# Optimization experiments

Hardware: AMD Instinct MI355X
Metric: run time of the kernel (lower is better)

Reference implementation:

```python
import jax, jax.numpy as jnp
import numpy as np
import math

E = 512; V = 8192; B = 32; T = 16; L = 4; FF = 2048; NH = 8; TEMP = 1.0


def setup_inputs() -> dict:
    key = jax.random.key(0)
    ks = jax.random.split(key, 16)
    s = 0.02
    nrm = lambda k, shape, sc=s: jax.random.normal(k, shape, jnp.float32) * sc
    d = {}
    d['encoder_state'] = nrm(ks[0], (1, B, E), 1.0)
    d['special_symbol'] = nrm(ks[1], (1, 1, E))
    d['embed_weight'] = nrm(ks[2], (V, E), E ** -0.5)
    d['out_w'] = nrm(ks[3], (V, E))
    d['out_b'] = jnp.zeros((V,), jnp.float32)
    u = jax.random.uniform(ks[4], (T, B, V), jnp.float32, 1e-6, 1.0 - 1e-6)
    d['gumbel'] = -jnp.log(-jnp.log(u))
    d['sa_qkv_w'] = nrm(ks[5], (L, 3 * E, E)); d['sa_qkv_b'] = jnp.zeros((L, 3 * E), jnp.float32)
    d['sa_out_w'] = nrm(ks[6], (L, E, E)); d['sa_out_b'] = jnp.zeros((L, E), jnp.float32)
    d['ca_qkv_w'] = nrm(ks[7], (L, 3 * E, E)); d['ca_qkv_b'] = jnp.zeros((L, 3 * E), jnp.float32)
    d['ca_out_w'] = nrm(ks[8], (L, E, E)); d['ca_out_b'] = jnp.zeros((L, E), jnp.float32)
    for i in (1, 2, 3):
        d['ln%d_g' % i] = jnp.ones((L, E), jnp.float32)
        d['ln%d_b' % i] = jnp.zeros((L, E), jnp.float32)
    d['w1'] = nrm(ks[9], (L, FF, E)); d['b1'] = jnp.zeros((L, FF), jnp.float32)
    d['w2'] = nrm(ks[10], (L, E, FF)); d['b2'] = jnp.zeros((L, E), jnp.float32)
    return d


def _ln(x, g, b):
    m = x.mean(-1, keepdims=True)
    v = ((x - m) ** 2).mean(-1, keepdims=True)
    return (x - m) / jnp.sqrt(v + 1e-5) * g + b


def _mha(q_in, kv_in, qkv_w, qkv_b, out_w, out_b, mask):
    # q_in: [Sq,B,E], kv_in: [Sk,B,E]; fused PyTorch-style in_proj
    hd = E // NH
    wq, wk, wv = jnp.split(qkv_w, 3, 0)
    bq, bk, bv = jnp.split(qkv_b, 3, 0)
    q = (q_in @ wq.T + bq).reshape(q_in.shape[0], -1, NH, hd)
    k = (kv_in @ wk.T + bk).reshape(kv_in.shape[0], -1, NH, hd)
    v = (kv_in @ wv.T + bv).reshape(kv_in.shape[0], -1, NH, hd)
    s = jnp.einsum('qbhd,kbhd->bhqk', q, k) / math.sqrt(hd)
    if mask is not None:
        s = s + mask
    a = jax.nn.softmax(s, -1)
    o = jnp.einsum('bhqk,kbhd->qbhd', a, v).reshape(q_in.shape[0], -1, E)
    return o @ out_w.T + out_b


def _forward(encoder_state, special_symbol, embed_weight, out_w, out_b, gumbel,
             sa_qkv_w, sa_qkv_b, sa_out_w, sa_out_b,
             ca_qkv_w, ca_qkv_b, ca_out_w, ca_out_b,
             ln1_g, ln1_b, ln2_g, ln2_b, ln3_g, ln3_b,
             w1, b1, w2, b2):
    bsz = encoder_state.shape[1]
    embed_scale = math.sqrt(E)
    inp = jnp.broadcast_to(special_symbol, (1, bsz, E))  # special start symbol
    seq_steps, distribs = [], []
    for step in range(T):
        t = step + 1
        mask = jnp.where(jnp.triu(jnp.ones((t, t), bool), 1), -jnp.inf, 0.0)
        x = inp
        for l in range(L):  # post-norm TransformerDecoderLayer, erf-gelu
            sa = _mha(x, x, sa_qkv_w[l], sa_qkv_b[l], sa_out_w[l], sa_out_b[l], mask)
            x = _ln(x + sa, ln1_g[l], ln1_b[l])
            ca = _mha(x, encoder_state, ca_qkv_w[l], ca_qkv_b[l], ca_out_w[l], ca_out_b[l], None)
            x = _ln(x + ca, ln2_g[l], ln2_b[l])
            ff = jax.nn.gelu(x @ w1[l].T + b1[l], approximate=False) @ w2[l].T + b2[l]
            x = _ln(x + ff, ln3_g[l], ln3_b[l])
        logits = x[-1] @ out_w.T + out_b  # [B,V], last position only
        distribs.append(jax.nn.softmax(logits, -1))
        sample = jax.nn.softmax((logits + gumbel[step]) / TEMP, -1)  # gumbel-softmax (training mode)
        seq_steps.append(sample)
        new_emb = (sample @ embed_weight) * embed_scale  # soft embedding lookup
        inp = jnp.concatenate([inp, new_emb[None]], 0)
    sequence = jnp.stack(seq_steps).transpose(1, 0, 2)  # [B,T,V]
    eos = jnp.zeros_like(sequence[:, :1, :]).at[:, :, 0].set(1.0)
    sequence = jnp.concatenate([sequence, eos], 1)  # [B,T+1,V]
    return sequence, jnp.stack(distribs)  # distribs: [T,B,V]


def reference(encoder_state, special_symbol, embed_weight, out_w, out_b, gumbel,
              sa_qkv_w, sa_qkv_b, sa_out_w, sa_out_b,
              ca_qkv_w, ca_qkv_b, ca_out_w, ca_out_b,
              ln1_g, ln1_b, ln2_g, ln2_b, ln3_g, ln3_b,
              w1, b1, w2, b2):
    return _forward(encoder_state, special_symbol, embed_weight, out_w, out_b, gumbel,
                    sa_qkv_w, sa_qkv_b, sa_out_w, sa_out_b,
                    ca_qkv_w, ca_qkv_b, ca_out_w, ca_out_b,
                    ln1_g, ln1_b, ln2_g, ln2_b, ln3_g, ln3_b,
                    w1, b1, w2, b2)
```

## Files before the change

### kernel.cpp

```cpp
#include <hip/hip_runtime.h>
#include <math.h>

#define BB 32
#define EE 512
#define VV 8192
#define TT 16
#define LL 4
#define FFD 2048
#define NHD 8
#define HDD 64
#define LDP 520
#define RWP 516
#define OLP 72
#define SCALE_EMB 22.627416997969522f

typedef __attribute__((ext_vector_type(8))) short bf16x8;
typedef __attribute__((ext_vector_type(4))) float f32x4;
typedef unsigned long long ull;

__device__ __forceinline__ f32x4 mfma16(bf16x8 a, bf16x8 b, f32x4 c){
  return __builtin_amdgcn_mfma_f32_16x16x32_bf16(a, b, c, 0, 0, 0);
}

__device__ __forceinline__ float wave_sum(float v){
// ... 35 lines not shown
        wt[(kk+2)*68 + fr] = v.z;
        wt[(kk+3)*68 + fr] = v.w;
      }
    }
    __syncthreads();
    const unsigned short* xr0 = xs + (bg*2)*EE + k0;
    const unsigned short* xr1 = xr0 + EE;
    #pragma unroll 8
    for (int k = 0; k < 64; k += 2){
      float w0[4], w1[4];
      *(float4*)w0 = *(const float4*)(wt + (k+0)*68 + fg*4);
      *(float4*)w1 = *(const float4*)(wt + (k+1)*68 + fg*4);
      float2 xv0 = bf2_to_f2(xr0 + k);
      float2 xv1 = bf2_to_f2(xr1 + k);
      #pragma unroll
      for (int i = 0; i < 4; ++i){
        acc[i][0] += w0[i]*xv0.x + w1[i]*xv0.y;
        acc[i][1] += w0[i]*xv1.x + w1[i]*xv1.y;
      }
    }
  }
}

__device__ __forceinline__ void stage_x_p(unsigned short* xs,
    const float* __restrict__ xraw, const float* __restrict__ ybuf,
    const float* __restrict__ g, const float* __restrict__ bt, int use_ln,
    float* __restrict__ xlnout){
  if (!use_ln){
    for (int i = threadIdx.x; i < BB*EE; i += 256){
      int r = i >> 9, c = i & 511;
      xs[r*LDP + c] = f_to_bf(xraw[i]);
    }
  } else {
    const int lane = threadIdx.x & 63, wv = threadIdx.x >> 6;
    for (int r = wv*8; r < wv*8 + 8; ++r){
      float vals[8]; float s = 0.f, s2 = 0.f;
      #pragma unroll
      for (int j = 0; j < 8; ++j){
        float v = ybuf[r*EE + lane + j*64];
        vals[j] = v; s += v; s2 += v*v;
      }
      s = wave_sum(s); s2 = wave_sum(s2);
      float m = s * (1.f/EE);
      float inv = rsqrtf(s2*(1.f/EE) - m*m + 1e-5f);
      #pragma unroll
      for (int j = 0; j < 8; ++j){
        int c = lane + j*64;
        float v = (vals[j]-m)*inv*g[c] + bt[c];
        xs[r*LDP + c] = f_to_bf(v);
        if (xlnout) xlnout[r*EE + c] = v;
      }
    }
  }
  __syncthreads();
}


__global__ __launch_bounds__(256) void k_init(const float* __restrict__ special,
    float* __restrict__ dseq, float* __restrict__ x, float* __restrict__ o2){
  int idx = blockIdx.x*256 + threadIdx.x;
  if (idx < BB*VV){
    int b = idx >> 13, v = idx & (VV-1);
    dseq[(size_t)b*((TT+1)*VV) + (size_t)TT*VV + v] = (v == 0) ? 1.f : 0.f;
  } else if (idx < BB*VV + BB*EE){
    int i = idx - BB*VV;
    x[i] = special[i & (EE-1)];
  } else if (idx < BB*VV + 2*BB*EE){
    o2[idx - BB*VV - BB*EE] = 0.f;
  }
}

__global__ __launch_bounds__(256) void k_penc(const float* __restrict__ enc,
    const float* __restrict__ w, const float* __restrict__ bias, float* __restrict__ venc){
  __shared__ unsigned short xs[BB*EE];
  __shared__ float wt[64*68];
  const int l = blockIdx.x >> 3, et = blockIdx.x & 7;
  for (int i = threadIdx.x; i < BB*EE; i += 256) xs[i] = f_to_bf(enc[i]);
  const int t = threadIdx.x, fg = t & 15, bg = t >> 4;
  const int f0 = et*64;
  const float* wl = w + (size_t)l*3*EE*EE + (size_t)(2*EE + f0)*EE;
  const float* bl = bias + l*3*EE + 2*EE + f0;
  float acc[4][2];
  #pragma unroll
  for (int i = 0; i < 4; ++i){ float bv = bl[fg*4+i]; acc[i][0] = bv; acc[i][1] = bv; }
  gemm_chunk(wl, EE, xs, wt, acc);
  #pragma unroll
  for (int i = 0; i < 4; ++i)
    #pragma unroll
    for (int j = 0; j < 2; ++j)
      venc[(size_t)l*BB*EE + (bg*2+j)*EE + f0 + fg*4 + i] = acc[i][j];
}
// ... 28 lines not shown
    ushort4 o;
    o.x = f_to_bf(v.x); o.y = f_to_bf(v.y); o.z = f_to_bf(v.z); o.w = f_to_bf(v.w);
    ((ushort4*)d)[i] = o;
  }
}

__global__ __launch_bounds__(256) void k_embT(const float* __restrict__ emb,
    unsigned short* __restrict__ eT){
  __shared__ unsigned short tl[64][68];
  const int vt = blockIdx.x >> 3, et = blockIdx.x & 7;
  const int v0 = vt*64, e0 = et*64;
  for (int i = threadIdx.x; i < 64*64; i += 256){
    int vv = i >> 6, ee = i & 63;
    tl[vv][ee] = f_to_bf(emb[(size_t)(v0+vv)*EE + e0 + ee]);
  }
  __syncthreads();
  for (int i = threadIdx.x; i < 64*64; i += 256){
    int ee = i >> 6, vv = i & 63;
    eT[(size_t)(e0+ee)*VV + v0 + vv] = tl[vv][ee];
  }
}


__global__ __launch_bounds__(256) void k_A(
    const float* __restrict__ x, const float* __restrict__ ybuf,
    const float* __restrict__ lng, const float* __restrict__ lnb, int use_ln,
    const unsigned short* __restrict__ Wb, const float* __restrict__ bias,
    const unsigned short* __restrict__ owb_l,
    float* __restrict__ kcl, float* __restrict__ vcl,
    float* __restrict__ xln, float* __restrict__ o2,
    int tpos, int tlen){
  __shared__ unsigned short xs[BB*LDP];
  __shared__ __align__(16) float qs[BB*68];
  __shared__ float att[BB*16];
  const int h = blockIdx.x;
  stage_x_p(xs, x, ybuf, lng, lnb, use_ln, (use_ln && h == 0) ? xln : nullptr);
  const int t = threadIdx.x, wv = t >> 6, lane = t & 63;
  const int lm = lane & 15, kg = lane >> 4;
  const unsigned short* b0r = xs + lm*LDP + kg*8;
  const unsigned short* b1r = xs + (lm+16)*LDP + kg*8;
  #pragma unroll
  for (int c = 0; c < 3; ++c){
    const int fbase = c*EE + h*64 + wv*16;
    const unsigned short* ar = Wb + (size_t)(fbase + lm)*EE + kg*8;
    f32x4 acc0 = {0.f,0.f,0.f,0.f}, acc1 = {0.f,0.f,0.f,0.f};
    #pragma unroll 4
    for (int ks = 0; ks < 16; ++ks){
      bf16x8 a  = *reinterpret_cast<const bf16x8*>(ar + ks*32);
      bf16x8 b0 = *reinterpret_cast<const bf16x8*>(b0r + ks*32);
      bf16x8 b1 = *reinterpret_cast<const bf16x8*>(b1r + ks*32);
      acc0 = mfma16(a, b0, acc0);
      acc1 = mfma16(a, b1, acc1);
    }
    #pragma unroll
    for (int r = 0; r < 4; ++r){
      const int frel = wv*16 + kg*4 + r;
      const float bv = bias[c*EE + h*64 + frel];
      float v0 = acc0[r] + bv, v1 = acc1[r] + bv;
      if (c == 0){
        qs[lm*68 + frel] = v0;
        qs[(lm+16)*68 + frel] = v1;
      } else if (c == 1){
        kcl[((lm*NHD + h)*TT + tpos)*HDD + frel] = v0;
        kcl[(((lm+16)*NHD + h)*TT + tpos)*HDD + frel] = v1;
      } else {
        vcl[((lm*NHD + h)*TT + tpos)*HDD + frel] = v0;
        vcl[(((lm+16)*NHD + h)*TT + tpos)*HDD + frel] = v1;
      }
    }
  }
  __syncthreads();
  #pragma unroll
  for (int pp = 0; pp < 2; ++pp){
    const int p = t + pp*256;
    const int b = p >> 4, j = p & 15;
    if (j < tlen){
      const float* qrow = qs + b*68;
      const float* krow = kcl + ((b*NHD + h)*TT + j)*HDD;
      float a = 0.f;
      #pragma unroll
      for (int d = 0; d < HDD; d += 4){
        float4 qv = *(const float4*)(qrow + d);
        float4 kv = *(const float4*)(krow + d);
        a += qv.x*kv.x + qv.y*kv.y + qv.z*kv.z + qv.w*kv.w;
      }
      att[b*16 + j] = a*0.125f;
    }
  }
  __syncthreads();
  if (t < 32){
    const int b = t;
    float m = -1e30f;
    for (int j = 0; j < tlen; ++j) m = fmaxf(m, att[b*16 + j]);
    float s = 0.f;
    for (int j = 0; j < tlen; ++j) s += __expf(att[b*16 + j] - m);
    float inv = 1.f/s;
    for (int j = 0; j < tlen; ++j) att[b*16 + j] = __expf(att[b*16 + j] - m)*inv;
  }
  __syncthreads();
  unsigned short* o_lds = (unsigned short*)qs;
  {
    const int b = t >> 3, d0 = (t & 7)*8;
    float acc[8];
    #pragma unroll
    for (int i = 0; i < 8; ++i) acc[i] = 0.f;
    const float* vrow = vcl + ((b*NHD + h)*TT)*HDD + d0;
    for (int j = 0; j < tlen; ++j){
      const float a = att[b*16 + j];
      float4 v0 = *(const float4*)(vrow + j*HDD);
      float4 v1 = *(const float4*)(vrow + j*HDD + 4);
      acc[0] += a*v0.x; acc[1] += a*v0.y; acc[2] += a*v0.z; acc[3] += a*v0.w;
      acc[4] += a*v1.x; acc[5] += a*v1.y; acc[6] += a*v1.z; acc[7] += a*v1.w;
    }
    *(ull*)(o_lds + b*OLP + d0)     = pkbf4(acc[0], acc[1], acc[2], acc[3]);
    *(ull*)(o_lds + b*OLP + d0 + 4) = pkbf4(acc[4], acc[5], acc[6], acc[7]);
  }
  __syncthreads();
  const unsigned short* ob0 = o_lds + lm*OLP + kg*8;
  const unsigned short* ob1 = o_lds + (lm+16)*OLP + kg*8;
  #pragma unroll
  for (int ft = 0; ft < 8; ++ft){
    const int f0 = wv*128 + ft*16;
    const unsigned short* ar = owb_l + (size_t)(f0 + lm)*EE + h*HDD + kg*8;
    f32x4 a0 = {0.f,0.f,0.f,0.f}, a1 = {0.f,0.f,0.f,0.f};
    #pragma unroll
    for (int ks = 0; ks < 2; ++ks){
      bf16x8 a  = *reinterpret_cast<const bf16x8*>(ar + ks*32);
      bf16x8 x0 = *reinterpret_cast<const bf16x8*>(ob0 + ks*32);
      bf16x8 x1 = *reinterpret_cast<const bf16x8*>(ob1 + ks*32);
      a0 = mfma16(a, x0, a0);
      a1 = mfma16(a, x1, a1);
    }
    #pragma unroll
    for (int r = 0; r < 4; ++r){
      const int f = f0 + kg*4 + r;
      atomicAdd(&o2[lm*EE + f], a0[r]);
      atomicAdd(&o2[(lm+16)*EE + f], a1[r]);
    }
  }
}

__global__ __launch_bounds__(256) void k_B(
    const float* __restrict__ o2, const float* __restrict__ resid,
    const float* __restrict__ ob, const float* __restrict__ cac,
    const float* __restrict__ g1, const float* __restrict__ b1g,
    const float* __restrict__ g2, const float* __restrict__ b2g,
    const float* __restrict__ b2bias,
    const unsigned short* __restrict__ w1b, const float* __restrict__ b1bias,
    unsigned short* __restrict__ Hb, float* __restrict__ ybuf){
  __shared__ unsigned short xs[BB*LDP];
  __shared__ __align__(16) float rawf[BB*RWP];
  const int t = threadIdx.x, blk = blockIdx.x;
  for (int i = t*4; i < BB*EE; i += 1024){
    const int r = i >> 9, c = i & 511;
    float4 a  = *(const float4*)(o2 + i);
    float4 rr = *(const float4*)(resid + i);
    float4 ov = *(const float4*)(ob + c);
    rawf[r*RWP + c]     = a.x + rr.x + ov.x;
    rawf[r*RWP + c + 1] = a.y + rr.y + ov.y;
    rawf[r*RWP + c + 2] = a.z + rr.z + ov.z;
    rawf[r*RWP + c + 3] = a.w + rr.w + ov.w;
  }
  __syncthreads();
  const int wv = t >> 6, lane = t & 63;
  const int lm = lane & 15, kg = lane >> 4;
  {
    float* yi = (blk == 0) ? ybuf : nullptr;
    const int c0 = lane*4, c1 = 256 + lane*4;
    for (int r = wv*8; r < wv*8 + 8; ++r){
      float v[8];
      *(float4*)(v+0) = *(const float4*)(rawf + r*RWP + c0);
      *(float4*)(v+4) = *(const float4*)(rawf + r*RWP + c1);
      float s = 0.f, s2 = 0.f;
      #pragma unroll
      for (int j = 0; j < 8; ++j){ s += v[j]; s2 += v[j]*v[j]; }
      s = wave_sum(s); s2 = wave_sum(s2);
      float m = s*(1.f/EE), inv = rsqrtf(s2*(1.f/EE) - m*m + 1e-5f);
      float4 ca0 = *(const float4*)(cac + (size_t)r*EE + c0);
      float4 ca1 = *(const float4*)(cac + (size_t)r*EE + c1);
      float nv[8]; float u = 0.f, u2 = 0.f;
      nv[0] = (v[0]-m)*inv*g1[c0+0] + b1g[c0+0] + ca0.x;
      nv[1] = (v[1]-m)*inv*g1[c0+1] + b1g[c0+1] + ca0.y;
      nv[2] = (v[2]-m)*inv*g1[c0+2] + b1g[c0+2] + ca0.z;
      nv[3] = (v[3]-m)*inv*g1[c0+3] + b1g[c0+3] + ca0.w;
      nv[4] = (v[4]-m)*inv*g1[c1+0] + b1g[c1+0] + ca1.x;
      nv[5] = (v[5]-m)*inv*g1[c1+1] + b1g[c1+1] + ca1.y;
      nv[6] = (v[6]-m)*inv*g1[c1+2] + b1g[c1+2] + ca1.z;
      nv[7] = (v[7]-m)*inv*g1[c1+3] + b1g[c1+3] + ca1.w;
      #pragma unroll
      for (int j = 0; j < 8; ++j){ u += nv[j]; u2 += nv[j]*nv[j]; }
      u = wave_sum(u); u2 = wave_sum(u2);
      float m2 = u*(1.f/EE), inv2 = rsqrtf(u2*(1.f/EE) - m2*m2 + 1e-5f);
      float o0 = (nv[0]-m2)*inv2*g2[c0+0] + b2g[c0+0];
      float o1 = (nv[1]-m2)*inv2*g2[c0+1] + b2g[c0+1];
      float o2v = (nv[2]-m2)*inv2*g2[c0+2] + b2g[c0+2];
      float o3 = (nv[3]-m2)*inv2*g2[c0+3] + b2g[c0+3];
      float o4 = (nv[4]-m2)*inv2*g2[c1+0] + b2g[c1+0];
      float o5 = (nv[5]-m2)*inv2*g2[c1+1] + b2g[c1+1];
      float o6 = (nv[6]-m2)*inv2*g2[c1+2] + b2g[c1+2];
      float o7 = (nv[7]-m2)*inv2*g2[c1+3] + b2g[c1+3];
      *(ull*)(xs + r*LDP + c0) = pkbf4(o0, o1, o2v, o3);
      *(ull*)(xs + r*LDP + c1) = pkbf4(o4, o5, o6, o7);
      if (yi){
        float4 w0, w1;
        w0.x = o0 + b2bias[c0+0]; w0.y = o1 + b2bias[c0+1];
        w0.z = o2v + b2bias[c0+2]; w0.w = o3 + b2bias[c0+3];
        w1.x = o4 + b2bias[c1+0]; w1.y = o5 + b2bias[c1+1];
        w1.z = o6 + b2bias[c1+2]; w1.w = o7 + b2bias[c1+3];
        *(float4*)(yi + (size_t)r*EE + c0) = w0;
        *(float4*)(yi + (size_t)r*EE + c1) = w1;
      }
    }
    __syncthreads();
  }
  {
    const int f0w = blk*64 + wv*16;
    const unsigned short* ar = w1b + (size_t)(f0w + lm)*EE + kg*8;
    const unsigned short* b0r = xs + lm*LDP + kg*8;
    const unsigned short* b1r = xs + (lm+16)*LDP + kg*8;
    f32x4 acc0 = {0.f,0.f,0.f,0.f}, acc1 = {0.f,0.f,0.f,0.f};
    #pragma unroll 4
    for (int ks = 0; ks < 16; ++ks){
      bf16x8 a  = *reinterpret_cast<const bf16x8*>(ar + ks*32);
      bf16x8 b0 = *reinterpret_cast<const bf16x8*>(b0r + ks*32);
      bf16x8 b1 = *reinterpret_cast<const bf16x8*>(b1r + ks*32);
      acc0 = mfma16(a, b0, acc0);
      acc1 = mfma16(a, b1, acc1);
    }
    const int fb = f0w + kg*4;
    float h0[4], h1[4];
    #pragma unroll
    for (int r = 0; r < 4; ++r){
      const float bv = b1bias[fb + r];
      float v0 = acc0[r] + bv, v1 = acc1[r] + bv;
      h0[r] = 0.5f*v0*(1.f + erff(v0*0.70710678118654752f));
      h1[r] = 0.5f*v1*(1.f + erff(v1*0.70710678118654752f));
    }
    *(ull*)(Hb + lm*FFD + fb)      = pkbf4(h0[0], h0[1], h0[2], h0[3]);
    *(ull*)(Hb + (lm+16)*FFD + fb) = pkbf4(h1[0], h1[1], h1[2], h1[3]);
  }
}

__global__ __launch_bounds__(256) void k_C(
    const unsigned short* __restrict__ Hb, const unsigned short* __restrict__ w2b,
    float* __restrict__ ybuf, float* __restrict__ o2z){
  __shared__ unsigned short xs[BB*LDP];
  const int t = threadIdx.x, blk = blockIdx.x;
  const int k0 = (blk >> 3)*512;
  for (int i = t*16; i < BB*512; i += 4096){
    int r = i >> 9, c = i & 511;
    const unsigned short* s = Hb + (size_t)r*FFD + k0 + c;
    ull* dst = (ull*)(xs + r*LDP + c);
    dst[0] = *(const ull*)s;      dst[1] = *(const ull*)(s+4);
    dst[2] = *(const ull*)(s+8);  dst[3] = *(const ull*)(s+12);
  }
  __syncthreads();
  const int wv = t >> 6, lane = t & 63;
  const int lm = lane & 15, kg = lane >> 4;
  const int f0w = (blk & 7)*64 + wv*16;
  const unsigned short* ar = w2b + (size_t)(f0w + lm)*FFD + k0 + kg*8;
  const unsigned short* b0r = xs + lm*LDP + kg*8;
  const unsigned short* b1r = xs + (lm+16)*LDP + kg*8;
  f32x4 acc0 = {0.f,0.f,0.f,0.f}, acc1 = {0.f,0.f,0.f,0.f};
  #pragma unroll 4
  for (int ks = 0; ks < 16; ++ks){
    bf16x8 a  = *reinterpret_cast<const bf16x8*>(ar + ks*32);
    bf16x8 b0 = *reinterpret_cast<const bf16x8*>(b0r + ks*32);
    bf16x8 b1 = *reinterpret_cast<const bf16x8*>(b1r + ks*32);
    acc0 = mfma16(a, b0, acc0);
    acc1 = mfma16(a, b1, acc1);
  }
  #pragma unroll
  for (int r = 0; r < 4; ++r){
    const int f = f0w + kg*4 + r;
    atomicAdd(&ybuf[lm*EE + f], acc0[r]);
    atomicAdd(&ybuf[(lm+16)*EE + f], acc1[r]);
  }
  float2 z; z.x = 0.f; z.y = 0.f;
  *(float2*)(o2z + blk*512 + t*2) = z;
}

__global__ __launch_bounds__(256) void k_logits_m(
    const float* __restrict__ ybuf, const float* __restrict__ lng, const float* __restrict__ lnb,
    const unsigned short* __restrict__ Wb, const float* __restrict__ bias,
    float* __restrict__ logits){
  __shared__ unsigned short xs[BB*LDP];
  stage_x_p(xs, nullptr, ybuf, lng, lnb, 1, nullptr);
  const int t = threadIdx.x, w = t >> 6, l = t & 63;
  const int lm = l & 15, kg = l >> 4;
  const int f0w = blockIdx.x*64 + w*16;
  const unsigned short* ar = Wb + (size_t)(f0w + lm)*EE + kg*8;
  const unsigned short* b0r = xs + lm*LDP + kg*8;
  const unsigned short* b1r = xs + (lm+16)*LDP + kg*8;
  f32x4 acc0 = {0.f,0.f,0.f,0.f}, acc1 = {0.f,0.f,0.f,0.f};
  #pragma unroll 4
  for (int ks = 0; ks < 16; ++ks){
    bf16x8 a  = *reinterpret_cast<const bf16x8*>(ar + ks*32);
    bf16x8 b0 = *reinterpret_cast<const bf16x8*>(b0r + ks*32);
    bf16x8 b1 = *reinterpret_cast<const bf16x8*>(b1r + ks*32);
    acc0 = mfma16(a, b0, acc0);
    acc1 = mfma16(a, b1, acc1);
  }
  #pragma unroll
  for (int r = 0; r < 4; ++r){
    const int f = f0w + kg*4 + r;
    const float bv = bias[f];
    logits[lm*VV + f]      = acc0[r] + bv;
    logits[(lm+16)*VV + f] = acc1[r] + bv;
  }
}

__global__ __launch_bounds__(256) void k_softmax(const float* __restrict__ logits,
    const float* __restrict__ gum, float* __restrict__ dseq, float* __restrict__ ddist,
    unsigned short* __restrict__ sbf, float* __restrict__ x, int step){
  const int b = blockIdx.x, t = threadIdx.x, lane = t & 63, wv = t >> 6;
  __shared__ float red[8];
  const float* lr = logits + (size_t)b*VV;
  const float* gr = gum + (size_t)b*VV;
  float m1 = -1e30f, m2 = -1e30f;
  for (int i = t; i < VV; i += 256){
    float l = lr[i];
    m1 = fmaxf(m1, l);
    m2 = fmaxf(m2, l + gr[i]);
  }
  for (int o = 32; o; o >>= 1){ m1 = fmaxf(m1, __shfl_down(m1,o)); m2 = fmaxf(m2, __shfl_down(m2,o)); }
  if (lane == 0){ red[wv] = m1; red[4+wv] = m2; }
  __syncthreads();
  m1 = fmaxf(fmaxf(red[0],red[1]), fmaxf(red[2],red[3]));
  m2 = fmaxf(fmaxf(red[4],red[5]), fmaxf(red[6],red[7]));
  __syncthreads();
  float s1 = 0.f, s2 = 0.f;
  for (int i = t; i < VV; i += 256){
    float l = lr[i];
    s1 += __expf(l - m1);
    s2 += __expf(l + gr[i] - m2);
  }
  for (int o = 32; o; o >>= 1){ s1 += __shfl_down(s1,o); s2 += __shfl_down(s2,o); }
  if (lane == 0){ red[wv] = s1; red[4+wv] = s2; }
  __syncthreads();
  s1 = red[0]+red[1]+red[2]+red[3];
  s2 = red[4]+red[5]+red[6]+red[7];
  float r1 = 1.f/s1, r2 = 1.f/s2;
  float* dq = dseq + (size_t)b*((TT+1)*VV) + (size_t)step*VV;
  float* dd = ddist + (size_t)b*VV;
  for (int i = t; i < VV; i += 256){
    float l = lr[i];
    dd[i] = __expf(l - m1)*r1;
    float qv = __expf(l + gr[i] - m2)*r2;
    dq[i] = qv;
    sbf[(size_t)b*VV + i] = f_to_bf(qv);
  }
  for (int i = t; i < EE; i += 256) x[b*EE + i] = 0.f;
}

__global__ __launch_bounds__(256) void k_embed_m(
    const unsigned short* __restrict__ eT, const unsigned short* __restrict__ sbf,
    float* __restrict__ x){
  const int t = threadIdx.x, w = t >> 6, l = t & 63;
  const int lm = l & 15, kg = l >> 4;
  const int e0w = (blockIdx.x & 7)*64 + w*16;
  const int v0 = (blockIdx.x >> 3)*1024;
  const unsigned short* ar  = eT + (size_t)(e0w + lm)*VV + v0 + kg*8;
  const unsigned short* b0r = sbf + (size_t)lm*VV + v0 + kg*8;
  const unsigned short* b1r = sbf + (size_t)(lm+16)*VV + v0 + kg*8;
  f32x4 acc0 = {0.f,0.f,0.f,0.f}, acc1 = {0.f,0.f,0.f,0.f};
  #pragma unroll 8
  for (int ks = 0; ks < 32; ++ks){
    bf16x8 a  = *reinterpret_cast<const bf16x8*>(ar + ks*32);
    bf16x8 b0 = *reinterpret_cast<const bf16x8*>(b0r + ks*32);
    bf16x8 b1 = *reinterpret_cast<const bf16x8*>(b1r + ks*32);
    acc0 = mfma16(a, b0, acc0);
    acc1 = mfma16(a, b1, acc1);
  }
  #pragma unroll
  for (int r = 0; r < 4; ++r){
    const int e = e0w + kg*4 + r;
    atomicAdd(&x[lm*EE + e], acc0[r]*SCALE_EMB);
    atomicAdd(&x[(lm+16)*EE + e], acc1[r]*SCALE_EMB);
  }
}

extern "C" void kernel_launch(void* const* d_in, const int* in_sizes, int n_in,
                              void* d_out, int out_size, void* d_ws, size_t ws_size,
                              hipStream_t stream){
  (void)in_sizes; (void)n_in; (void)out_size; (void)ws_size;
  const float* enc  = (const float*)d_in[0];
  const float* spec = (const float*)d_in[1];
  const float* embw = (const float*)d_in[2];
  const float* outw = (const float*)d_in[3];
  const float* outb = (const float*)d_in[4];
  const float* gumb = (const float*)d_in[5];
  const float* saqw = (const float*)d_in[6];
  const float* saqb = (const float*)d_in[7];
  const float* saow = (const float*)d_in[8];
  const float* saob = (const float*)d_in[9];
  const float* caqw = (const float*)d_in[10];
  const float* caqb = (const float*)d_in[11];
  const float* caow = (const float*)d_in[12];
  const float* caob = (const float*)d_in[13];
  const float* l1g  = (const float*)d_in[14];
  const float* l1b  = (const float*)d_in[15];
  const float* l2g  = (const float*)d_in[16];
  const float* l2b  = (const float*)d_in[17];
  const float* l3g  = (const float*)d_in[18];
  const float* l3b  = (const float*)d_in[19];
  const float* w1   = (const float*)d_in[20];
  const float* b1   = (const float*)d_in[21];
  const float* w2   = (const float*)d_in[22];
  const float* b2   = (const float*)d_in[23];

  float* dout = (float*)d_out;
  float* dseq = dout;
  float* ddistbase = dout + (size_t)BB*(TT+1)*VV;

  unsigned char* p = (unsigned char*)d_ws;
  auto alloc = [&](size_t bytes) -> void* {
    void* r = (void*)p; p += (bytes + 255) & ~(size_t)255; return r;
  };
  float* x      = (float*)alloc(BB*EE*4);
  float* y      = (float*)alloc(BB*EE*4);
  float* xln    = (float*)alloc(BB*EE*4);
  float* o2     = (float*)alloc(BB*EE*4);
  float* logits = (float*)alloc((size_t)BB*VV*4);
  float* venc   = (float*)alloc((size_t)LL*BB*EE*4);
  float* cac    = (float*)alloc((size_t)LL*BB*EE*4);
  float* kcache = (float*)alloc((size_t)LL*BB*EE*TT*4);
  float* vcache = (float*)alloc((size_t)LL*BB*EE*TT*4);
  unsigned short* Hb    = (unsigned short*)alloc(BB*FFD*2);
  unsigned short* sbf   = (unsigned short*)alloc((size_t)BB*VV*2);
  unsigned short* wqkvb = (unsigned short*)alloc((size_t)LL*3*EE*EE*2);
  unsigned short* owb   = (unsigned short*)alloc((size_t)LL*EE*EE*2);
  unsigned short* w1b   = (unsigned short*)alloc((size_t)LL*FFD*EE*2);
  unsigned short* w2b   = (unsigned short*)alloc((size_t)LL*FFD*EE*2);
  unsigned short* outwb = (unsigned short*)alloc((size_t)VV*EE*2);
  unsigned short* eTb   = (unsigned short*)alloc((size_t)EE*VV*2);

  k_init<<<1152, 256, 0, stream>>>(spec, dseq, x, o2);
  k_penc<<<32, 256, 0, stream>>>(enc, caqw, caqb, venc);
  k_pca<<<32, 256, 0, stream>>>(venc, caow, caob, cac);
  k_cvt<<<(LL*3*EE*EE/4 + 255)/256, 256, 0, stream>>>(saqw, wqkvb, LL*3*EE*EE/4);
  k_cvt<<<(LL*EE*EE/4 + 255)/256, 256, 0, stream>>>(saow, owb, LL*EE*EE/4);
  k_cvt<<<(LL*FFD*EE/4 + 255)/256, 256, 0, stream>>>(w1, w1b, LL*FFD*EE/4);
  k_cvt<<<(LL*FFD*EE/4 + 255)/256, 256, 0, stream>>>(w2, w2b, LL*FFD*EE/4);
  k_cvt<<<(VV*EE/4 + 255)/256, 256, 0, stream>>>(outw, outwb, VV*EE/4);
  k_embT<<<1024, 256, 0, stream>>>(embw, eTb);

  for (int step = 0; step < TT; ++step){
    const int tpos = step, tlen = step + 1;
    for (int l = 0; l < LL; ++l){
      const int use_ln = (l > 0);
      const float* lg = l3g + (use_ln ? (l-1)*EE : 0);
      const float* lb = l3b + (use_ln ? (l-1)*EE : 0);
      float* kcl = kcache + (size_t)l*BB*EE*TT;
      float* vcl = vcache + (size_t)l*BB*EE*TT;
      const float* resid = use_ln ? xln : x;
      k_A<<<NHD, 256, 0, stream>>>(x, y, lg, lb, use_ln,
          wqkvb + (size_t)l*3*EE*EE, saqb + (size_t)l*3*EE,
          owb + (size_t)l*EE*EE, kcl, vcl, xln, o2, tpos, tlen);
      k_B<<<32, 256, 0, stream>>>(o2, resid, saob + (size_t)l*EE,
          cac + (size_t)l*BB*EE,
          l1g + l*EE, l1b + l*EE, l2g + l*EE, l2b + l*EE, b2 + l*EE,
          w1b + (size_t)l*FFD*EE, b1 + l*FFD, Hb, y);
      k_C<<<32, 256, 0, stream>>>(Hb, w2b + (size_t)l*EE*FFD, y, o2);
    }
    k_logits_m<<<128, 256, 0, stream>>>(y, l3g + 3*EE, l3b + 3*EE, outwb, outb, logits);
    k_softmax<<<32, 256, 0, stream>>>(logits, gumb + (size_t)step*BB*VV, dseq,
        ddistbase + (size_t)step*BB*VV, sbf, x, step);
    k_embed_m<<<64, 256, 0, stream>>>(eTb, sbf, x);
  }
}
```

Before: 4.543 ms.

## Fuse FFN kernels into one, double-buffer y/o2, and widen blocks to 512 threads

```diff
diff --git a/kernel.cpp b/kernel.cpp
--- a/kernel.cpp
+++ b/kernel.cpp
@@ -81,18 +81,19 @@
   }
 }
 
-__device__ __forceinline__ void stage_x_p(unsigned short* xs,
+__device__ __forceinline__ void stage_x_512(unsigned short* xs,
     const float* __restrict__ xraw, const float* __restrict__ ybuf,
     const float* __restrict__ g, const float* __restrict__ bt, int use_ln,
     float* __restrict__ xlnout){
   if (!use_ln){
-    for (int i = threadIdx.x; i < BB*EE; i += 256){
+    for (int i = threadIdx.x*4; i < BB*EE; i += 2048){
+      float4 v = *(const float4*)(xraw + i);
       int r = i >> 9, c = i & 511;
-      xs[r*LDP + c] = f_to_bf(xraw[i]);
+      *(ull*)(xs + r*LDP + c) = pkbf4(v.x, v.y, v.z, v.w);
     }
   } else {
     const int lane = threadIdx.x & 63, wv = threadIdx.x >> 6;
-    for (int r = wv*8; r < wv*8 + 8; ++r){
+    for (int r = wv*4; r < wv*4 + 4; ++r){
       float vals[8]; float s = 0.f, s2 = 0.f;
       #pragma unroll
       for (int j = 0; j < 8; ++j){
@@ -116,16 +117,23 @@
 
 
 __global__ __launch_bounds__(256) void k_init(const float* __restrict__ special,
-    float* __restrict__ dseq, float* __restrict__ x, float* __restrict__ o2){
+    float* __restrict__ dseq, float* __restrict__ x,
+    float* __restrict__ o2a, float* __restrict__ o2b,
+    float* __restrict__ y0, float* __restrict__ y1){
   int idx = blockIdx.x*256 + threadIdx.x;
   if (idx < BB*VV){
     int b = idx >> 13, v = idx & (VV-1);
     dseq[(size_t)b*((TT+1)*VV) + (size_t)TT*VV + v] = (v == 0) ? 1.f : 0.f;
   } else if (idx < BB*VV + BB*EE){
-    int i = idx - BB*VV;
-    x[i] = special[i & (EE-1)];
+    x[idx - BB*VV] = special[idx & (EE-1)];
   } else if (idx < BB*VV + 2*BB*EE){
-    o2[idx - BB*VV - BB*EE] = 0.f;
+    o2a[idx - BB*VV - BB*EE] = 0.f;
+  } else if (idx < BB*VV + 3*BB*EE){
+    o2b[idx - BB*VV - 2*BB*EE] = 0.f;
+  } else if (idx < BB*VV + 4*BB*EE){
+    y0[idx - BB*VV - 3*BB*EE] = 0.f;
+  } else if (idx < BB*VV + 5*BB*EE){
+    y1[idx - BB*VV - 4*BB*EE] = 0.f;
   }
 }
 
@@ -200,7 +208,7 @@
 }
 
 
-__global__ __launch_bounds__(256) void k_A(
+__global__ __launch_bounds__(512) void k_A(
     const float* __restrict__ x, const float* __restrict__ ybuf,
     const float* __restrict__ lng, const float* __restrict__ lnb, int use_ln,
     const unsigned short* __restrict__ Wb, const float* __restrict__ bias,
@@ -212,46 +220,47 @@
   __shared__ __align__(16) float qs[BB*68];
   __shared__ float att[BB*16];
   const int h = blockIdx.x;
-  stage_x_p(xs, x, ybuf, lng, lnb, use_ln, (use_ln && h == 0) ? xln : nullptr);
+  stage_x_512(xs, x, ybuf, lng, lnb, use_ln, (use_ln && h == 0) ? xln : nullptr);
   const int t = threadIdx.x, wv = t >> 6, lane = t & 63;
   const int lm = lane & 15, kg = lane >> 4;
   const unsigned short* b0r = xs + lm*LDP + kg*8;
   const unsigned short* b1r = xs + (lm+16)*LDP + kg*8;
-  #pragma unroll
-  for (int c = 0; c < 3; ++c){
-    const int fbase = c*EE + h*64 + wv*16;
-    const unsigned short* ar = Wb + (size_t)(fbase + lm)*EE + kg*8;
-    f32x4 acc0 = {0.f,0.f,0.f,0.f}, acc1 = {0.f,0.f,0.f,0.f};
-    #pragma unroll 4
-    for (int ks = 0; ks < 16; ++ks){
-      bf16x8 a  = *reinterpret_cast<const bf16x8*>(ar + ks*32);
-      bf16x8 b0 = *reinterpret_cast<const bf16x8*>(b0r + ks*32);
-      bf16x8 b1 = *reinterpret_cast<const bf16x8*>(b1r + ks*32);
-      acc0 = mfma16(a, b0, acc0);
-      acc1 = mfma16(a, b1, acc1);
-    }
-    #pragma unroll
-    for (int r = 0; r < 4; ++r){
-      const int frel = wv*16 + kg*4 + r;
-      const float bv = bias[c*EE + h*64 + frel];
-      float v0 = acc0[r] + bv, v1 = acc1[r] + bv;
-      if (c == 0){
-        qs[lm*68 + frel] = v0;
-        qs[(lm+16)*68 + frel] = v1;
-      } else if (c == 1){
-        kcl[((lm*NHD + h)*TT + tpos)*HDD + frel] = v0;
-        kcl[(((lm+16)*NHD + h)*TT + tpos)*HDD + frel] = v1;
-      } else {
-        vcl[((lm*NHD + h)*TT + tpos)*HDD + frel] = v0;
-        vcl[(((lm+16)*NHD + h)*TT + tpos)*HDD + frel] = v1;
-      }
-    }
-  }
-  __syncthreads();
-  #pragma unroll
-  for (int pp = 0; pp < 2; ++pp){
-    const int p = t + pp*256;
-    const int b = p >> 4, j = p & 15;
+  if (wv < 6){
+    const int c = wv >> 1, half = wv & 1;
+    #pragma unroll
+    for (int ft = 0; ft < 2; ++ft){
+      const int frel_t = (half*2 + ft)*16;
+      const unsigned short* ar = Wb + (size_t)(c*EE + h*64 + frel_t + lm)*EE + kg*8;
+      f32x4 acc0 = {0.f,0.f,0.f,0.f}, acc1 = {0.f,0.f,0.f,0.f};
+      #pragma unroll 4
+      for (int ks = 0; ks < 16; ++ks){
+        bf16x8 a  = *reinterpret_cast<const bf16x8*>(ar + ks*32);
+        bf16x8 b0 = *reinterpret_cast<const bf16x8*>(b0r + ks*32);
+        bf16x8 b1 = *reinterpret_cast<const bf16x8*>(b1r + ks*32);
+        acc0 = mfma16(a, b0, acc0);
+        acc1 = mfma16(a, b1, acc1);
+      }
+      #pragma unroll
+      for (int r = 0; r < 4; ++r){
+        const int frel = frel_t + kg*4 + r;
+        const float bv = bias[c*EE + h*64 + frel];
+        float v0 = acc0[r] + bv, v1 = acc1[r] + bv;
+        if (c == 0){
+          qs[lm*68 + frel] = v0;
+          qs[(lm+16)*68 + frel] = v1;
+        } else if (c == 1){
+          kcl[((lm*NHD + h)*TT + tpos)*HDD + frel] = v0;
+          kcl[(((lm+16)*NHD + h)*TT + tpos)*HDD + frel] = v1;
+        } else {
+          vcl[((lm*NHD + h)*TT + tpos)*HDD + frel] = v0;
+          vcl[(((lm+16)*NHD + h)*TT + tpos)*HDD + frel] = v1;
+        }
+      }
+    }
+  }
+  __syncthreads();
+  {
+    const int b = t >> 4, j = t & 15;
     if (j < tlen){
       const float* qrow = qs + b*68;
       const float* krow = kcl + ((b*NHD + h)*TT + j)*HDD;
@@ -278,27 +287,24 @@
   __syncthreads();
   unsigned short* o_lds = (unsigned short*)qs;
   {
-    const int b = t >> 3, d0 = (t & 7)*8;
-    float acc[8];
-    #pragma unroll
-    for (int i = 0; i < 8; ++i) acc[i] = 0.f;
+    const int b = t >> 4, d0 = (t & 15)*4;
+    float acc[4];
+    #pragma unroll
+    for (int i = 0; i < 4; ++i) acc[i] = 0.f;
     const float* vrow = vcl + ((b*NHD + h)*TT)*HDD + d0;
     for (int j = 0; j < tlen; ++j){
       const float a = att[b*16 + j];
-      float4 v0 = *(const float4*)(vrow + j*HDD);
-      float4 v1 = *(const float4*)(vrow + j*HDD + 4);
-      acc[0] += a*v0.x; acc[1] += a*v0.y; acc[2] += a*v0.z; acc[3] += a*v0.w;
-      acc[4] += a*v1.x; acc[5] += a*v1.y; acc[6] += a*v1.z; acc[7] += a*v1.w;
-    }
-    *(ull*)(o_lds + b*OLP + d0)     = pkbf4(acc[0], acc[1], acc[2], acc[3]);
-    *(ull*)(o_lds + b*OLP + d0 + 4) = pkbf4(acc[4], acc[5], acc[6], acc[7]);
+      float4 v = *(const float4*)(vrow + j*HDD);
+      acc[0] += a*v.x; acc[1] += a*v.y; acc[2] += a*v.z; acc[3] += a*v.w;
+    }
+    *(ull*)(o_lds + b*OLP + d0) = pkbf4(acc[0], acc[1], acc[2], acc[3]);
   }
   __syncthreads();
   const unsigned short* ob0 = o_lds + lm*OLP + kg*8;
   const unsigned short* ob1 = o_lds + (lm+16)*OLP + kg*8;
   #pragma unroll
-  for (int ft = 0; ft < 8; ++ft){
-    const int f0 = wv*128 + ft*16;
+  for (int ft = 0; ft < 4; ++ft){
+    const int f0 = wv*64 + ft*16;
     const unsigned short* ar = owb_l + (size_t)(f0 + lm)*EE + h*HDD + kg*8;
     f32x4 a0 = {0.f,0.f,0.f,0.f}, a1 = {0.f,0.f,0.f,0.f};
     #pragma unroll
@@ -318,20 +324,22 @@
   }
 }
 
-__global__ __launch_bounds__(256) void k_B(
-    const float* __restrict__ o2, const float* __restrict__ resid,
+__global__ __launch_bounds__(512) void k_BC(
+    const float* __restrict__ o2buf, const float* __restrict__ resid,
     const float* __restrict__ ob, const float* __restrict__ cac,
     const float* __restrict__ g1, const float* __restrict__ b1g,
     const float* __restrict__ g2, const float* __restrict__ b2g,
     const float* __restrict__ b2bias,
     const unsigned short* __restrict__ w1b, const float* __restrict__ b1bias,
-    unsigned short* __restrict__ Hb, float* __restrict__ ybuf){
+    const unsigned short* __restrict__ w2b,
+    float* __restrict__ ycur, float* __restrict__ yzero, float* __restrict__ o2zero){
   __shared__ unsigned short xs[BB*LDP];
   __shared__ __align__(16) float rawf[BB*RWP];
+  __shared__ unsigned short Hs[BB*OLP];
   const int t = threadIdx.x, blk = blockIdx.x;
-  for (int i = t*4; i < BB*EE; i += 1024){
+  for (int i = t*4; i < BB*EE; i += 2048){
     const int r = i >> 9, c = i & 511;
-    float4 a  = *(const float4*)(o2 + i);
+    float4 a  = *(const float4*)(o2buf + i);
     float4 rr = *(const float4*)(resid + i);
     float4 ov = *(const float4*)(ob + c);
     rawf[r*RWP + c]     = a.x + rr.x + ov.x;
@@ -343,9 +351,8 @@
   const int wv = t >> 6, lane = t & 63;
   const int lm = lane & 15, kg = lane >> 4;
   {
-    float* yi = (blk == 0) ? ybuf : nullptr;
     const int c0 = lane*4, c1 = 256 + lane*4;
-    for (int r = wv*8; r < wv*8 + 8; ++r){
+    for (int r = wv*4; r < wv*4 + 4; ++r){
       float v[8];
       *(float4*)(v+0) = *(const float4*)(rawf + r*RWP + c0);
       *(float4*)(v+4) = *(const float4*)(rawf + r*RWP + c1);
@@ -379,182 +386,180 @@
       float o7 = (nv[7]-m2)*inv2*g2[c1+3] + b2g[c1+3];
       *(ull*)(xs + r*LDP + c0) = pkbf4(o0, o1, o2v, o3);
       *(ull*)(xs + r*LDP + c1) = pkbf4(o4, o5, o6, o7);
-      if (yi){
-        float4 w0, w1;
-        w0.x = o0 + b2bias[c0+0]; w0.y = o1 + b2bias[c0+1];
-        w0.z = o2v + b2bias[c0+2]; w0.w = o3 + b2bias[c0+3];
-        w1.x = o4 + b2bias[c1+0]; w1.y = o5 + b2bias[c1+1];
-        w1.z = o6 + b2bias[c1+2]; w1.w = o7 + b2bias[c1+3];
-        *(float4*)(yi + (size_t)r*EE + c0) = w0;
-        *(float4*)(yi + (size_t)r*EE + c1) = w1;
-      }
-    }
-    __syncthreads();
-  }
+      if ((c0 >> 4) == blk){
+        atomicAdd(&ycur[(size_t)r*EE + c0+0], o0 + b2bias[c0+0]);
+        atomicAdd(&ycur[(size_t)r*EE + c0+1], o1 + b2bias[c0+1]);
+        atomicAdd(&ycur[(size_t)r*EE + c0+2], o2v + b2bias[c0+2]);
+        atomicAdd(&ycur[(size_t)r*EE + c0+3], o3 + b2bias[c0+3]);
+      }
+      if ((c1 >> 4) == blk){
+        atomicAdd(&ycur[(size_t)r*EE + c1+0], o4 + b2bias[c1+0]);
+        atomicAdd(&ycur[(size_t)r*EE + c1+1], o5 + b2bias[c1+1]);
+        atomicAdd(&ycur[(size_t)r*EE + c1+2], o6 + b2bias[c1+2]);
+        atomicAdd(&ycur[(size_t)r*EE + c1+3], o7 + b2bias[c1+3]);
+      }
+    }
+  }
+  __syncthreads();
   {
-    const int f0w = blk*64 + wv*16;
+    const int ftile = wv & 3, rh = wv >> 2;
+    const int f0w = blk*64 + ftile*16;
     const unsigned short* ar = w1b + (size_t)(f0w + lm)*EE + kg*8;
-    const unsigned short* b0r = xs + lm*LDP + kg*8;
-    const unsigned short* b1r = xs + (lm+16)*LDP + kg*8;
-    f32x4 acc0 = {0.f,0.f,0.f,0.f}, acc1 = {0.f,0.f,0.f,0.f};
+    const unsigned short* br = xs + (lm + rh*16)*LDP + kg*8;
+    f32x4 acc = {0.f,0.f,0.f,0.f};
     #pragma unroll 4
     for (int ks = 0; ks < 16; ++ks){
-      bf16x8 a  = *reinterpret_cast<const bf16x8*>(ar + ks*32);
-      bf16x8 b0 = *reinterpret_cast<const bf16x8*>(b0r + ks*32);
-      bf16x8 b1 = *reinterpret_cast<const bf16x8*>(b1r + ks*32);
-      acc0 = mfma16(a, b0, acc0);
-      acc1 = mfma16(a, b1, acc1);
-    }
-    const int fb = f0w + kg*4;
-    float h0[4], h1[4];
+      bf16x8 a = *reinterpret_cast<const bf16x8*>(ar + ks*32);
+      bf16x8 b = *reinterpret_cast<const bf16x8*>(br + ks*32);
+      acc = mfma16(a, b, acc);
+    }
+    const int fbrel = ftile*16 + kg*4;
+    float hh[4];
     #pragma unroll
     for (int r = 0; r < 4; ++r){
-      const float bv = b1bias[fb + r];
-      float v0 = acc0[r] + bv, v1 = acc1[r] + bv;
-      h0[r] = 0.5f*v0*(1.f + erff(v0*0.70710678118654752f));
-      h1[r] = 0.5f*v1*(1.f + erff(v1*0.70710678118654752f));
-    }
-    *(ull*)(Hb + lm*FFD + fb)      = pkbf4(h0[0], h0[1], h0[2], h0[3]);
-    *(ull*)(Hb + (lm+16)*FFD + fb) = pkbf4(h1[0], h1[1], h1[2], h1[3]);
-  }
-}
-
-__global__ __launch_bounds__(256) void k_C(
-    const unsigned short* __restrict__ Hb, const unsigned short* __restrict__ w2b,
-    float* __restrict__ ybuf, float* __restrict__ o2z){
-  __shared__ unsigned short xs[BB*LDP];
-  const int t = threadIdx.x, blk = blockIdx.x;
-  const int k0 = (blk >> 3)*512;
-  for (int i = t*16; i < BB*512; i += 4096){
-    int r = i >> 9, c = i & 511;
-    const unsigned short* s = Hb + (size_t)r*FFD + k0 + c;
-    ull* dst = (ull*)(xs + r*LDP + c);
-    dst[0] = *(const ull*)s;      dst[1] = *(const ull*)(s+4);
-    dst[2] = *(const ull*)(s+8);  dst[3] = *(const ull*)(s+12);
-  }
-  __syncthreads();
-  const int wv = t >> 6, lane = t & 63;
-  const int lm = lane & 15, kg = lane >> 4;
-  const int f0w = (blk & 7)*64 + wv*16;
-  const unsigned short* ar = w2b + (size_t)(f0w + lm)*FFD + k0 + kg*8;
-  const unsigned short* b0r = xs + lm*LDP + kg*8;
-  const unsigned short* b1r = xs + (lm+16)*LDP + kg*8;
-  f32x4 acc0 = {0.f,0.f,0.f,0.f}, acc1 = {0.f,0.f,0.f,0.f};
-  #pragma unroll 4
-  for (int ks = 0; ks < 16; ++ks){
-    bf16x8 a  = *reinterpret_cast<const bf16x8*>(ar + ks*32);
-    bf16x8 b0 = *reinterpret_cast<const bf16x8*>(b0r + ks*32);
-    bf16x8 b1 = *reinterpret_cast<const bf16x8*>(b1r + ks*32);
-    acc0 = mfma16(a, b0, acc0);
-    acc1 = mfma16(a, b1, acc1);
-  }
-  #pragma unroll
-  for (int r = 0; r < 4; ++r){
-    const int f = f0w + kg*4 + r;
-    atomicAdd(&ybuf[lm*EE + f], acc0[r]);
-    atomicAdd(&ybuf[(lm+16)*EE + f], acc1[r]);
-  }
-  float2 z; z.x = 0.f; z.y = 0.f;
-  *(float2*)(o2z + blk*512 + t*2) = z;
-}
-
-__global__ __launch_bounds__(256) void k_logits_m(
+      const float bv = b1bias[blk*64 + fbrel + r];
+      float vv = acc[r] + bv;
+      hh[r] = 0.5f*vv*(1.f + erff(vv*0.70710678118654752f));
+    }
+    *(ull*)(Hs + (lm + rh*16)*OLP + fbrel) = pkbf4(hh[0], hh[1], hh[2], hh[3]);
+  }
+  __syncthreads();
+  {
+    const unsigned short* hb0 = Hs + lm*OLP + kg*8;
+    const unsigned short* hb1 = Hs + (lm+16)*OLP + kg*8;
+    #pragma unroll
+    for (int et = 0; et < 4; ++et){
+      const int e0 = (wv*4 + et)*16;
+      const unsigned short* ar = w2b + (size_t)(e0 + lm)*FFD + blk*64 + kg*8;
+      f32x4 a0 = {0.f,0.f,0.f,0.f}, a1 = {0.f,0.f,0.f,0.f};
+      #pragma unroll
+      for (int ks = 0; ks < 2; ++ks){
+        bf16x8 a  = *reinterpret_cast<const bf16x8*>(ar + ks*32);
+        bf16x8 h0 = *reinterpret_cast<const bf16x8*>(hb0 + ks*32);
+        bf16x8 h1 = *reinterpret_cast<const bf16x8*>(hb1 + ks*32);
+        a0 = mfma16(a, h0, a0);
+        a1 = mfma16(a, h1, a1);
+      }
+      #pragma unroll
+      for (int r = 0; r < 4; ++r){
+        const int e = e0 + kg*4 + r;
+        atomicAdd(&ycur[lm*EE + e], a0[r]);
+        atomicAdd(&ycur[(lm+16)*EE + e], a1[r]);
+      }
+    }
+  }
+  yzero[blk*512 + t] = 0.f;
+  o2zero[blk*512 + t] = 0.f;
+}
+
+__global__ __launch_bounds__(512) void k_logits_m(
     const float* __restrict__ ybuf, const float* __restrict__ lng, const float* __restrict__ lnb,
     const unsigned short* __restrict__ Wb, const float* __restrict__ bias,
     float* __restrict__ logits){
   __shared__ unsigned short xs[BB*LDP];
-  stage_x_p(xs, nullptr, ybuf, lng, lnb, 1, nullptr);
-  const int t = threadIdx.x, w = t >> 6, l = t & 63;
-  const int lm = l & 15, kg = l >> 4;
-  const int f0w = blockIdx.x*64 + w*16;
+  stage_x_512(xs, nullptr, ybuf, lng, lnb, 1, nullptr);
+  const int t = threadIdx.x, wv = t >> 6, lane = t & 63;
+  const int lm = lane & 15, kg = lane >> 4;
+  const int ftile = wv & 3, rh = wv >> 2;
+  const int f0w = blockIdx.x*64 + ftile*16;
   const unsigned short* ar = Wb + (size_t)(f0w + lm)*EE + kg*8;
-  const unsigned short* b0r = xs + lm*LDP + kg*8;
-  const unsigned short* b1r = xs + (lm+16)*LDP + kg*8;
-  f32x4 acc0 = {0.f,0.f,0.f,0.f}, acc1 = {0.f,0.f,0.f,0.f};
+  const unsigned short* br = xs + (lm + rh*16)*LDP + kg*8;
+  f32x4 acc = {0.f,0.f,0.f,0.f};
   #pragma unroll 4
   for (int ks = 0; ks < 16; ++ks){
-    bf16x8 a  = *reinterpret_cast<const bf16x8*>(ar + ks*32);
-    bf16x8 b0 = *reinterpret_cast<const bf16x8*>(b0r + ks*32);
-    bf16x8 b1 = *reinterpret_cast<const bf16x8*>(b1r + ks*32);
-    acc0 = mfma16(a, b0, acc0);
-    acc1 = mfma16(a, b1, acc1);
+    bf16x8 a = *reinterpret_cast<const bf16x8*>(ar + ks*32);
+    bf16x8 b = *reinterpret_cast<const bf16x8*>(br + ks*32);
+    acc = mfma16(a, b, acc);
   }
   #pragma unroll
   for (int r = 0; r < 4; ++r){
     const int f = f0w + kg*4 + r;
-    const float bv = bias[f];
-    logits[lm*VV + f]      = acc0[r] + bv;
-    logits[(lm+16)*VV + f] = acc1[r] + bv;
-  }
-}
-
-__global__ __launch_bounds__(256) void k_softmax(const float* __restrict__ logits,
+    logits[(size_t)(lm + rh*16)*VV + f] = acc[r] + bias[f];
+  }
+}
+
+__global__ __launch_bounds__(512) void k_softmax(const float* __restrict__ logits,
     const float* __restrict__ gum, float* __restrict__ dseq, float* __restrict__ ddist,
     unsigned short* __restrict__ sbf, float* __restrict__ x, int step){
   const int b = blockIdx.x, t = threadIdx.x, lane = t & 63, wv = t >> 6;
-  __shared__ float red[8];
+  __shared__ float red[16];
   const float* lr = logits + (size_t)b*VV;
   const float* gr = gum + (size_t)b*VV;
+  float lv[16], gv[16];
+  #pragma unroll
+  for (int g4 = 0; g4 < 4; ++g4){
+    const int i0 = t*4 + g4*2048;
+    float4 l4 = *(const float4*)(lr + i0);
+    float4 g4v = *(const float4*)(gr + i0);
+    lv[g4*4+0]=l4.x; lv[g4*4+1]=l4.y; lv[g4*4+2]=l4.z; lv[g4*4+3]=l4.w;
+    gv[g4*4+0]=g4v.x; gv[g4*4+1]=g4v.y; gv[g4*4+2]=g4v.z; gv[g4*4+3]=g4v.w;
+  }
   float m1 = -1e30f, m2 = -1e30f;
-  for (int i = t; i < VV; i += 256){
-    float l = lr[i];
-    m1 = fmaxf(m1, l);
-    m2 = fmaxf(m2, l + gr[i]);
+  #pragma unroll
+  for (int j = 0; j < 16; ++j){
+    m1 = fmaxf(m1, lv[j]);
+    m2 = fmaxf(m2, lv[j] + gv[j]);
   }
   for (int o = 32; o; o >>= 1){ m1 = fmaxf(m1, __shfl_down(m1,o)); m2 = fmaxf(m2, __shfl_down(m2,o)); }
-  if (lane == 0){ red[wv] = m1; red[4+wv] = m2; }
-  __syncthreads();
-  m1 = fmaxf(fmaxf(red[0],red[1]), fmaxf(red[2],red[3]));
-  m2 = fmaxf(fmaxf(red[4],red[5]), fmaxf(red[6],red[7]));
+  if (lane == 0){ red[wv] = m1; red[8+wv] = m2; }
+  __syncthreads();
+  m1 = red[0]; m2 = red[8];
+  #pragma unroll
+  for (int j = 1; j < 8; ++j){ m1 = fmaxf(m1, red[j]); m2 = fmaxf(m2, red[8+j]); }
   __syncthreads();
   float s1 = 0.f, s2 = 0.f;
-  for (int i = t; i < VV; i += 256){
-    float l = lr[i];
-    s1 += __expf(l - m1);
-    s2 += __expf(l + gr[i] - m2);
+  #pragma unroll
+  for (int j = 0; j < 16; ++j){
+    s1 += __expf(lv[j] - m1);
+    s2 += __expf(lv[j] + gv[j] - m2);
   }
   for (int o = 32; o; o >>= 1){ s1 += __shfl_down(s1,o); s2 += __shfl_down(s2,o); }
-  if (lane == 0){ red[wv] = s1; red[4+wv] = s2; }
-  __syncthreads();
-  s1 = red[0]+red[1]+red[2]+red[3];
-  s2 = red[4]+red[5]+red[6]+red[7];
+  if (lane == 0){ red[wv] = s1; red[8+wv] = s2; }
+  __syncthreads();
+  s1 = 0.f; s2 = 0.f;
+  #pragma unroll
+  for (int j = 0; j < 8; ++j){ s1 += red[j]; s2 += red[8+j]; }
   float r1 = 1.f/s1, r2 = 1.f/s2;
   float* dq = dseq + (size_t)b*((TT+1)*VV) + (size_t)step*VV;
   float* dd = ddist + (size_t)b*VV;
-  for (int i = t; i < VV; i += 256){
-    float l = lr[i];
-    dd[i] = __expf(l - m1)*r1;
-    float qv = __expf(l + gr[i] - m2)*r2;
-    dq[i] = qv;
-    sbf[(size_t)b*VV + i] = f_to_bf(qv);
-  }
-  for (int i = t; i < EE; i += 256) x[b*EE + i] = 0.f;
-}
-
-__global__ __launch_bounds__(256) void k_embed_m(
+  #pragma unroll
+  for (int g4 = 0; g4 < 4; ++g4){
+    const int i0 = t*4 + g4*2048;
+    float4 ddv, dqv;
+    ddv.x = __expf(lv[g4*4+0]-m1)*r1; ddv.y = __expf(lv[g4*4+1]-m1)*r1;
+    ddv.z = __expf(lv[g4*4+2]-m1)*r1; ddv.w = __expf(lv[g4*4+3]-m1)*r1;
+    dqv.x = __expf(lv[g4*4+0]+gv[g4*4+0]-m2)*r2;
+    dqv.y = __expf(lv[g4*4+1]+gv[g4*4+1]-m2)*r2;
+    dqv.z = __expf(lv[g4*4+2]+gv[g4*4+2]-m2)*r2;
+    dqv.w = __expf(lv[g4*4+3]+gv[g4*4+3]-m2)*r2;
+    *(float4*)(dd + i0) = ddv;
+    *(float4*)(dq + i0) = dqv;
+    *(ull*)(sbf + (size_t)b*VV + i0) = pkbf4(dqv.x, dqv.y, dqv.z, dqv.w);
+  }
+  x[b*EE + t] = 0.f;
+}
+
+__global__ __launch_bounds__(512) void k_embed_m(
     const unsigned short* __restrict__ eT, const unsigned short* __restrict__ sbf,
     float* __restrict__ x){
-  const int t = threadIdx.x, w = t >> 6, l = t & 63;
-  const int lm = l & 15, kg = l >> 4;
-  const int e0w = (blockIdx.x & 7)*64 + w*16;
-  const int v0 = (blockIdx.x >> 3)*1024;
-  const unsigned short* ar  = eT + (size_t)(e0w + lm)*VV + v0 + kg*8;
-  const unsigned short* b0r = sbf + (size_t)lm*VV + v0 + kg*8;
-  const unsigned short* b1r = sbf + (size_t)(lm+16)*VV + v0 + kg*8;
-  f32x4 acc0 = {0.f,0.f,0.f,0.f}, acc1 = {0.f,0.f,0.f,0.f};
-  #pragma unroll 8
-  for (int ks = 0; ks < 32; ++ks){
-    bf16x8 a  = *reinterpret_cast<const bf16x8*>(ar + ks*32);
-    bf16x8 b0 = *reinterpret_cast<const bf16x8*>(b0r + ks*32);
-    bf16x8 b1 = *reinterpret_cast<const bf16x8*>(b1r + ks*32);
-    acc0 = mfma16(a, b0, acc0);
-    acc1 = mfma16(a, b1, acc1);
+  const int t = threadIdx.x, wv = t >> 6, lane = t & 63;
+  const int lm = lane & 15, kg = lane >> 4;
+  const int etile = wv & 3, rh = wv >> 2;
+  const int e0 = (blockIdx.x & 7)*64 + etile*16;
+  const int v0 = (blockIdx.x >> 3)*512;
+  const unsigned short* ar = eT + (size_t)(e0 + lm)*VV + v0 + kg*8;
+  const unsigned short* br = sbf + (size_t)(lm + rh*16)*VV + v0 + kg*8;
+  f32x4 acc = {0.f,0.f,0.f,0.f};
+  #pragma unroll 4
+  for (int ks = 0; ks < 16; ++ks){
+    bf16x8 a = *reinterpret_cast<const bf16x8*>(ar + ks*32);
+    bf16x8 b = *reinterpret_cast<const bf16x8*>(br + ks*32);
+    acc = mfma16(a, b, acc);
   }
   #pragma unroll
   for (int r = 0; r < 4; ++r){
-    const int e = e0w + kg*4 + r;
-    atomicAdd(&x[lm*EE + e], acc0[r]*SCALE_EMB);
-    atomicAdd(&x[(lm+16)*EE + e], acc1[r]*SCALE_EMB);
+    const int e = e0 + kg*4 + r;
+    atomicAdd(&x[(lm + rh*16)*EE + e], acc[r]*SCALE_EMB);
   }
 }
 
@@ -596,15 +601,16 @@
     void* r = (void*)p; p += (bytes + 255) & ~(size_t)255; return r;
   };
   float* x      = (float*)alloc(BB*EE*4);
-  float* y      = (float*)alloc(BB*EE*4);
+  float* y0     = (float*)alloc(BB*EE*4);
+  float* y1     = (float*)alloc(BB*EE*4);
   float* xln    = (float*)alloc(BB*EE*4);
-  float* o2     = (float*)alloc(BB*EE*4);
+  float* o2a    = (float*)alloc(BB*EE*4);
+  float* o2b    = (float*)alloc(BB*EE*4);
   float* logits = (float*)alloc((size_t)BB*VV*4);
   float* venc   = (float*)alloc((size_t)LL*BB*EE*4);
   float* cac    = (float*)alloc((size_t)LL*BB*EE*4);
   float* kcache = (float*)alloc((size_t)LL*BB*EE*TT*4);
   float* vcache = (float*)alloc((size_t)LL*BB*EE*TT*4);
-  unsigned short* Hb    = (unsigned short*)alloc(BB*FFD*2);
   unsigned short* sbf   = (unsigned short*)alloc((size_t)BB*VV*2);
   unsigned short* wqkvb = (unsigned short*)alloc((size_t)LL*3*EE*EE*2);
   unsigned short* owb   = (unsigned short*)alloc((size_t)LL*EE*EE*2);
@@ -613,7 +619,7 @@
   unsigned short* outwb = (unsigned short*)alloc((size_t)VV*EE*2);
   unsigned short* eTb   = (unsigned short*)alloc((size_t)EE*VV*2);
 
-  k_init<<<1152, 256, 0, stream>>>(spec, dseq, x, o2);
+  k_init<<<1344, 256, 0, stream>>>(spec, dseq, x, o2a, o2b, y0, y1);
   k_penc<<<32, 256, 0, stream>>>(enc, caqw, caqb, venc);
   k_pca<<<32, 256, 0, stream>>>(venc, caow, caob, cac);
   k_cvt<<<(LL*3*EE*EE/4 + 255)/256, 256, 0, stream>>>(saqw, wqkvb, LL*3*EE*EE/4);
@@ -623,27 +629,30 @@
   k_cvt<<<(VV*EE/4 + 255)/256, 256, 0, stream>>>(outw, outwb, VV*EE/4);
   k_embT<<<1024, 256, 0, stream>>>(embw, eTb);
 
+  float* yb[2]  = { y0, y1 };
+  float* o2p[2] = { o2a, o2b };
+
   for (int step = 0; step < TT; ++step){
     const int tpos = step, tlen = step + 1;
     for (int l = 0; l < LL; ++l){
       const int use_ln = (l > 0);
+      const int par = l & 1, opp = par ^ 1;
       const float* lg = l3g + (use_ln ? (l-1)*EE : 0);
       const float* lb = l3b + (use_ln ? (l-1)*EE : 0);
       float* kcl = kcache + (size_t)l*BB*EE*TT;
       float* vcl = vcache + (size_t)l*BB*EE*TT;
-      const float* resid = use_ln ? xln : x;
-      k_A<<<NHD, 256, 0, stream>>>(x, y, lg, lb, use_ln,
+      k_A<<<NHD, 512, 0, stream>>>(x, yb[opp], lg, lb, use_ln,
           wqkvb + (size_t)l*3*EE*EE, saqb + (size_t)l*3*EE,
-          owb + (size_t)l*EE*EE, kcl, vcl, xln, o2, tpos, tlen);
-      k_B<<<32, 256, 0, stream>>>(o2, resid, saob + (size_t)l*EE,
-          cac + (size_t)l*BB*EE,
+          owb + (size_t)l*EE*EE, kcl, vcl, xln, o2p[par], tpos, tlen);
+      k_BC<<<32, 512, 0, stream>>>(o2p[par], use_ln ? xln : x,
+          saob + (size_t)l*EE, cac + (size_t)l*BB*EE,
           l1g + l*EE, l1b + l*EE, l2g + l*EE, l2b + l*EE, b2 + l*EE,
-          w1b + (size_t)l*FFD*EE, b1 + l*FFD, Hb, y);
-      k_C<<<32, 256, 0, stream>>>(Hb, w2b + (size_t)l*EE*FFD, y, o2);
-    }
-    k_logits_m<<<128, 256, 0, stream>>>(y, l3g + 3*EE, l3b + 3*EE, outwb, outb, logits);
-    k_softmax<<<32, 256, 0, stream>>>(logits, gumb + (size_t)step*BB*VV, dseq,
+          w1b + (size_t)l*FFD*EE, b1 + l*FFD, w2b + (size_t)l*EE*FFD,
+          yb[par], yb[opp], o2p[opp]);
+    }
+    k_logits_m<<<128, 512, 0, stream>>>(yb[1], l3g + 3*EE, l3b + 3*EE, outwb, outb, logits);
+    k_softmax<<<32, 512, 0, stream>>>(logits, gumb + (size_t)step*BB*VV, dseq,
         ddistbase + (size_t)step*BB*VV, sbf, x, step);
-    k_embed_m<<<64, 256, 0, stream>>>(eTb, sbf, x);
-  }
-}
+    k_embed_m<<<128, 512, 0, stream>>>(eTb, sbf, x);
+  }
+}
```

Result: faster. 4.143 ms (-8.8%).
